# Performance work log

Measured on AMD Instinct MI355X. Metric: run time of the kernel, lower is better.

## Reference

```python
import jax, jax.numpy as jnp
import numpy as np

BIG = 1e9      # stand-in for +inf (keeps fp math/grad clean)
ALPHA = 0.5    # distillation weight from __init__
EPS = 1e-12


def _pairwise_dist(X):
    # Euclidean cdist: [N, d] -> [N, N]
    sq = jnp.sum(X * X, axis=1)
    D2 = sq[:, None] + sq[None, :] - 2.0 * (X @ X.T)
    return jnp.sqrt(jnp.maximum(D2, EPS))


def _h0_diagram(X):
    """0-dim persistence diagram from pairwise distances (single-linkage).
    births are 0, deaths are the sorted MST edge weights (Prim's algorithm).
    Returns [N-1, 2] (birth, death) pairs."""
    D = _pairwise_dist(X)           # [N, N]
    n = D.shape[0]
    visited0 = jnp.zeros(n, dtype=bool).at[0].set(True)

    def step(carry, _):
        dist, visited = carry       # dist: min distance from tree to each node
        masked = jnp.where(visited, BIG, dist)
        j = jnp.argmin(masked)
        w = masked[j]               # MST edge weight added this step
        visited = visited.at[j].set(True)
        dist = jnp.minimum(dist, D[j])
        return (dist, visited), w

    (_, _), deaths = jax.lax.scan(step, (D[0], visited0), None, length=n - 1)
    deaths = jnp.sort(deaths)
    return jnp.stack([jnp.zeros_like(deaths), deaths], axis=-1)  # [N-1, 2]


def reference(student_repr, teacher_repr, student_edges, teacher_edges):
    # representation MSE
    repr_loss = jnp.mean((student_repr - teacher_repr) ** 2)
    # topological distillation: MSE between H0 persistence diagrams
    # (edges are unused: persistence is computed from the feature distance matrix,
    #  matching ph.compute_from_distance(features) in the source)
    diag_s = _h0_diagram(student_repr)
    diag_t = _h0_diagram(teacher_repr)
    topo_loss = jnp.mean((diag_s - diag_t) ** 2)
    total = ALPHA * repr_loss + (1.0 - ALPHA) * topo_loss
    return total, repr_loss, topo_loss


def setup_inputs() -> dict:
    key = jax.random.key(0)
    k1, k2, k3, k4 = jax.random.split(key, 4)
    N, d, E = 4096, 128, 131072
    return {
        "student_repr": jax.random.normal(k1, (N, d), dtype=jnp.float32),
        "teacher_repr": jax.random.normal(k2, (N, d), dtype=jnp.float32),
        "student_edges": jax.random.randint(k3, (2, E), 0, N, dtype=jnp.int64)
        if jax.config.jax_enable_x64 else jax.random.randint(k3, (2, E), 0, N).astype(jnp.int32),
        "teacher_edges": jax.random.randint(k4, (2, E), 0, N, dtype=jnp.int64)
        if jax.config.jax_enable_x64 else jax.random.randint(k4, (2, E), 0, N).astype(jnp.int32),
    }
```

## Files before the change

kernel.cpp:

```cpp
#include <hip/hip_runtime.h>
#include <hip/hip_fp16.h>

#define N_NODES 4096
#define DIMS 128

typedef __attribute__((ext_vector_type(8))) short short8;
typedef __attribute__((ext_vector_type(4))) float f32x4;

static constexpr float BIGF = 1e9f;
static constexpr float EPSF = 1e-12f;
static constexpr unsigned long long KEY_INF = ~0ull;
static constexpr unsigned U32_INF = 0xFFFFFFFFu;


__device__ inline unsigned short f32_to_bf16(float f) {
    unsigned u = __float_as_uint(f);
    unsigned r = (u + 0x7FFFu + ((u >> 16) & 1u)) >> 16;
    return (unsigned short)r;
}

__device__ inline float half_bits_to_f32(unsigned short b) {
    __half h;
    __builtin_memcpy(&h, &b, 2);
    return __half2float(h);
}

__device__ inline unsigned u32min(unsigned a, unsigned b) { return a < b ? a : b; }

__device__ inline unsigned long long u64min(unsigned long long a, unsigned long long b) {
    return a < b ? a : b;
}

__device__ inline unsigned long long shfl_xor_u64(unsigned long long v, int m) {
    int lo = __shfl_xor((int)(unsigned)(v & 0xFFFFFFFFull), m);
    int hi = __shfl_xor((int)(unsigned)(v >> 32), m);
    return ((unsigned long long)(unsigned)hi << 32) | (unsigned)lo;
}

__device__ inline unsigned wave_min_u32(unsigned v) {
    #pragma unroll
    for (int s = 32; s; s >>= 1) v = u32min(v, (unsigned)__shfl_xor((int)v, s));
    return v;
}

__device__ inline float block_reduce_sum_256(float v) {
    __shared__ float s[4];
    __syncthreads();
    #pragma unroll
    for (int off = 32; off; off >>= 1) v += __shfl_xor(v, off);
    if ((threadIdx.x & 63) == 0) s[threadIdx.x >> 6] = v;
    __syncthreads();
    return s[0] + s[1] + s[2] + s[3];
}

__global__ __launch_bounds__(256) void prep_kernel(const float* __restrict__ S,
                                                   const float* __restrict__ T,
                                                   unsigned short* __restrict__ X16s,
                                                   unsigned short* __restrict__ X16t,
                                                   float* __restrict__ sqs,
                                                   float* __restrict__ sqt,
                                                   float* __restrict__ partials,
                                                   unsigned short* __restrict__ comp0,
                                                   unsigned long long* __restrict__ best_row,
                                                   unsigned* __restrict__ cnt,
                                                   unsigned* __restrict__ done,
                                                   unsigned* __restrict__ sctl) {
    const int t = threadIdx.x;
    const int gid = blockIdx.x * 256 + t;
    if (gid < 2 * N_NODES) {
        comp0[gid] = (unsigned short)(gid & (N_NODES - 1));
        best_row[gid] = KEY_INF;
    }
    if (gid < 2) { cnt[gid] = 0; done[gid] = 0; }
    if (gid == 0) sctl[0] = 0;

    const int wave = t >> 6, lane = t & 63;
    const int row = blockIdx.x * 8 + wave * 2 + (lane >> 5);
    const int c4 = (lane & 31) * 4;
    const size_t off = (size_t)row * DIMS + c4;
    float4 a = *(const float4*)&S[off];
    float4 b = *(const float4*)&T[off];
    float sa = a.x * a.x + a.y * a.y + a.z * a.z + a.w * a.w;
    float sb = b.x * b.x + b.y * b.y + b.z * b.z + b.w * b.w;
    #pragma unroll
    for (int m = 16; m; m >>= 1) { sa += __shfl_xor(sa, m); sb += __shfl_xor(sb, m); }
    if ((lane & 31) == 0) { sqs[row] = sa; sqt[row] = sb; }
    ushort4 oa, ob;
    oa.x = f32_to_bf16(a.x); oa.y = f32_to_bf16(a.y);
    oa.z = f32_to_bf16(a.z); oa.w = f32_to_bf16(a.w);
    ob.x = f32_to_bf16(b.x); ob.y = f32_to_bf16(b.y);
    ob.z = f32_to_bf16(b.z); ob.w = f32_to_bf16(b.w);
    *(ushort4*)&X16s[off] = oa;
    *(ushort4*)&X16t[off] = ob;
    float dx = a.x - b.x, dy = a.y - b.y, dz = a.z - b.z, dw = a.w - b.w;
    float rs = block_reduce_sum_256(dx * dx + dy * dy + dz * dz + dw * dw);
    if (t == 0) partials[blockIdx.x] = rs;
}

__global__ __launch_bounds__(256) void dist_kernel(const unsigned short* __restrict__ X16s,
                                                   const unsigned short* __restrict__ X16t,
                                                   const float* __restrict__ sqs,
                                                   const float* __restrict__ sqt,
                                                   __half* __restrict__ Ds,
                                                   __half* __restrict__ Dt,
                                                   unsigned long long* __restrict__ best_row,
                                                   unsigned* __restrict__ rowtile) {
    const int bi = blockIdx.y * 64;
    const int bj = blockIdx.x * 64;
    if (bj < bi) return;
    const int m = blockIdx.z;
    const unsigned short* __restrict__ X16 = m ? X16t : X16s;
    const float* __restrict__ sq = m ? sqt : sqs;
    unsigned short* __restrict__ D = (unsigned short*)(m ? Dt : Ds);
    unsigned long long* br = best_row + m * N_NODES;
    unsigned* rt = rowtile + (size_t)m * N_NODES * 64;

    __shared__ __align__(16) unsigned short Abuf[64 * 128];
    __shared__ __align__(16) unsigned short Bbuf[64 * 128];
    __shared__ unsigned colminLDS[4 * 64];
    unsigned short* tile16 = Abuf;

    const int t = threadIdx.x;

    #pragma unroll
    for (int p = 0; p < 4; p++) {
        int f = t + p * 256;
        int r = f >> 4, c8 = f & 15;
        int slot = c8 ^ (r & 7);
        uint4 va = *(const uint4*)&X16[(size_t)(bi + r) * DIMS + c8 * 8];
        *(uint4*)&Abuf[r * 128 + slot * 8] = va;
        uint4 vb = *(const uint4*)&X16[(size_t)(bj + r) * DIMS + c8 * 8];
        *(uint4*)&Bbuf[r * 128 + slot * 8] = vb;
    }
    __syncthreads();

    const int wave = t >> 6, lane = t & 63;
    const int l15 = lane & 15, kg = lane >> 4;

    const int rowA = wave * 16 + l15;
    short8 afrag[4];
    #pragma unroll
    for (int s = 0; s < 4; s++) {
        int c8 = s * 4 + kg;
        int slot = c8 ^ (rowA & 7);
        afrag[s] = *(const short8*)&Abuf[rowA * 128 + slot * 8];
    }
    __syncthreads();

    f32x4 acc[4] = {};
    #pragma unroll
    for (int n = 0; n < 4; n++) {
        const int rowB = n * 16 + l15;
        #pragma unroll
        for (int s = 0; s < 4; s++) {
            int c8 = s * 4 + kg;
            int slot = c8 ^ (rowB & 7);
            short8 bfrag = *(const short8*)&Bbuf[rowB * 128 + slot * 8];
            acc[n] = __builtin_amdgcn_mfma_f32_16x16x32_bf16(afrag[s], bfrag, acc[n], 0, 0, 0);
        }
    }

    const int r0 = wave * 16 + kg * 4;
    float sqi[4];
    #pragma unroll
    for (int rr = 0; rr < 4; rr++) sqi[rr] = sq[bi + r0 + rr];

    unsigned rowmin[4] = {U32_INF, U32_INF, U32_INF, U32_INF};
    unsigned colmin[4] = {U32_INF, U32_INF, U32_INF, U32_INF};
    #pragma unroll
    for (int n = 0; n < 4; n++) {
        const int col = bj + n * 16 + l15;
        const float sqj = sq[col];
        #pragma unroll
        for (int rr = 0; rr < 4; rr++) {
            float d2 = sqi[rr] + sqj - 2.0f * acc[n][rr];
            float dd = sqrtf(fmaxf(d2, EPSF));
            unsigned hb = (unsigned)__half_as_ushort(__float2half(dd));
            const int cc = n * 16 + l15;
            const int R = r0 + rr;
            tile16[R * 72 + ((((cc >> 3) ^ (R & 7)) << 3) | (cc & 7))] = (unsigned short)hb;
            if ((bi + R) != col) {
                rowmin[rr] = u32min(rowmin[rr], (hb << 12) | (unsigned)col);
                colmin[n]  = u32min(colmin[n],  (hb << 12) | (unsigned)R);
            }
        }
    }
    #pragma unroll
    for (int rr = 0; rr < 4; rr++) {
        unsigned k = rowmin[rr];
        #pragma unroll
        for (int s = 8; s; s >>= 1) k = u32min(k, (unsigned)__shfl_xor((int)k, s));
        if (l15 == 0) {
            const unsigned row = (unsigned)(bi + r0 + rr);
            rt[(size_t)row * 64 + (bj >> 6)] = k;
            unsigned j = k & 0xFFFu, d16 = k >> 12;
            unsigned a = row < j ? row : j, b2 = row < j ? j : row;
            atomicMin(&br[row],
                ((unsigned long long)d16 << 24) | ((unsigned long long)a << 12) | b2);
        }
    }
    #pragma unroll
    for (int n = 0; n < 4; n++) {
        unsigned k = colmin[n];
        k = u32min(k, (unsigned)__shfl_xor((int)k, 16));
        k = u32min(k, (unsigned)__shfl_xor((int)k, 32));
        if (kg == 0) colminLDS[wave * 64 + n * 16 + l15] = k;
    }
    __syncthreads();

    #pragma unroll
    for (int q = 0; q < 2; q++) {
        int lin = t * 2 + q;
        int r = lin >> 3, k8 = lin & 7;
        uint4 v = *(const uint4*)&tile16[r * 72 + ((k8 ^ (r & 7)) << 3)];
        *(uint4*)&D[(size_t)(bi + r) * N_NODES + bj + k8 * 8] = v;
    }
    if (bi != bj) {
        #pragma unroll
        for (int q = 0; q < 2; q++) {
            int lin = t * 2 + q;
            int c = lin >> 3, r8 = lin & 7;
            const int csl = ((c >> 3) << 3);
            unsigned w[4];
            #pragma unroll
            for (int h = 0; h < 4; h++) {
                int R0 = r8 * 8 + h * 2;
                int R1 = R0 + 1;
                unsigned lo = tile16[R0 * 72 + ((((c >> 3) ^ (R0 & 7)) << 3) | (c & 7))];
                unsigned hi = tile16[R1 * 72 + ((((c >> 3) ^ (R1 & 7)) << 3) | (c & 7))];
                w[h] = lo | (hi << 16);
            }
            uint4 v = make_uint4(w[0], w[1], w[2], w[3]);
            *(uint4*)&D[(size_t)(bj + c) * N_NODES + bi + r8 * 8] = v;
        }
        if (t < 64) {
            unsigned k = colminLDS[t];
            k = u32min(k, colminLDS[64 + t]);
            k = u32min(k, colminLDS[128 + t]);
            k = u32min(k, colminLDS[192 + t]);
            unsigned d16 = k >> 12, lrow = k & 0xFFFu;
            rt[(size_t)(bj + t) * 64 + (bi >> 6)] = (d16 << 12) | (unsigned)(bi + lrow);
            unsigned long long key64 = ((unsigned long long)d16 << 24) |
                ((unsigned long long)(bi + lrow) << 12) | (unsigned)(bj + t);
            atomicMin(&br[bj + t], key64);
        }
    }
}

__global__ __launch_bounds__(1024) void boruvka_merge2(
        const unsigned short* __restrict__ comp_in,
        unsigned short* __restrict__ comp_out,
        const unsigned long long* __restrict__ bc_in,
        unsigned long long* __restrict__ bc_out,
        const unsigned long long* __restrict__ best_row,
        unsigned short* __restrict__ wlist,
        unsigned* __restrict__ wcount,
        float* __restrict__ deaths,
        unsigned* __restrict__ cnt,
        unsigned* __restrict__ done) {
    const int m = blockIdx.x;
    if (done[m]) return;
    const unsigned short* cin = comp_in + m * N_NODES;
    const unsigned long long* bi = bc_in + m * N_NODES;
    const unsigned long long* br = best_row + m * N_NODES;
    float* dth = deaths + m * N_NODES;

    __shared__ unsigned short s_mc[N_NODES];
    __shared__ unsigned short s_mp[N_NODES];
    __shared__ unsigned long long s_bc[N_NODES];
    __shared__ unsigned s_wc;

    const int t = threadIdx.x;
    for (int i = t; i < N_NODES; i += 1024) {
        s_mc[i] = cin[i];
        s_mp[i] = (unsigned short)i;
        s_bc[i] = bi[i];
    }
    if (t == 0) s_wc = 0;
    __syncthreads();

    for (int i = t; i < N_NODES; i += 1024) {
        unsigned long long k = s_bc[i];
        if (k != KEY_INF) {
            unsigned canon = (unsigned)(k & 0xFFFFFFu);
            unsigned a = canon >> 12, b = canon & 0xFFFu;
            unsigned ca = s_mc[a], cb = s_mc[b];
            unsigned other = (ca == (unsigned)i) ? cb : ca;
            s_mp[i] = (unsigned short)other;
            bool mutual = (s_bc[other] == k);
            if (!mutual || (unsigned)i < other) {
                unsigned idx = atomicAdd(&cnt[m], 1u);
                dth[idx] = half_bits_to_f32((unsigned short)(k >> 24));
            }
        }
    }
    __syncthreads();

    unsigned nv[4];
    #pragma unroll
    for (int q = 0; q < 4; q++) {
        unsigned i = (unsigned)(t + q * 1024);
        unsigned p = s_mp[i], pp = s_mp[p];
        nv[q] = (pp == i) ? (i < p ? i : p) : p;
    }
    __syncthreads();
    #pragma unroll
    for (int q = 0; q < 4; q++) s_mp[t + q * 1024] = (unsigned short)nv[q];
    __syncthreads();

    #pragma unroll
    for (int q = 0; q < 4; q++) {
        unsigned rt = (unsigned)(t + q * 1024);
        unsigned p = s_mp[rt];
        while (p != rt) { rt = p; p = s_mp[rt]; }
        nv[q] = rt;
    }
    __syncthreads();
    #pragma unroll
    for (int q = 0; q < 4; q++) s_mp[t + q * 1024] = (unsigned short)nv[q];
    __syncthreads();

    #pragma unroll
    for (int q = 0; q < 4; q++) {
        int i = t + q * 1024;
        s_mc[i] = s_mp[s_mc[i]];
        s_bc[i] = KEY_INF;
    }
    __syncthreads();

    for (int i = t; i < N_NODES; i += 1024) {
        unsigned long long k = br[i];
        if (k != KEY_INF) {
            unsigned canon = (unsigned)(k & 0xFFFFFFu);
            unsigned a = canon >> 12, b = canon & 0xFFFu;
            unsigned j = (a == (unsigned)i) ? b : a;
            unsigned ci = s_mc[i];
            if (s_mc[j] != ci) {
                atomicMin(&s_bc[ci], k);
            } else {
                unsigned idx = atomicAdd(&s_wc, 1u);
                wlist[m * N_NODES + idx] = (unsigned short)i;
            }
        }
    }
    __syncthreads();

    for (int i = t; i < N_NODES; i += 1024) {
        comp_out[m * N_NODES + i] = s_mc[i];
        bc_out[m * N_NODES + i] = s_bc[i];
    }
    if (t == 0) {
        wcount[m] = s_wc;
        unsigned c = atomicAdd(&cnt[m], 0u);
        if (c >= N_NODES - 1) done[m] = 1u;
    }
}

__global__ __launch_bounds__(1024) void boruvka_scanw(
        const unsigned short* __restrict__ D0,
        const unsigned short* __restrict__ D1,
        const unsigned short* __restrict__ comp16,
        const unsigned short* __restrict__ wlist,
        const unsigned* __restrict__ wcount,
        unsigned* __restrict__ rowtile,
        unsigned long long* __restrict__ best_row,
        unsigned long long* __restrict__ bc_scan,
        const unsigned* __restrict__ done) {
    const int m = blockIdx.y;
    if (done[m]) return;
    const unsigned count = wcount[m];
    if (blockIdx.x * 16 >= count) return;

    const unsigned short* __restrict__ D = m ? D1 : D0;
    const unsigned short* cm = comp16 + m * N_NODES;
    unsigned* rt = rowtile + (size_t)m * N_NODES * 64;
    unsigned long long* br = best_row + m * N_NODES;
    unsigned long long* bc = bc_scan + m * N_NODES;

    __shared__ __align__(16) unsigned short s_c16[N_NODES];

    const int t = threadIdx.x;
    {
        uint2 v = ((const uint2*)cm)[t];
        *(uint2*)&s_c16[t * 4] = v;
    }
    __syncthreads();

    const int wave = t >> 6, lane = t & 63;
    const unsigned idx = blockIdx.x * 16 + wave;
    if (idx >= count) return;
    const int r = (int)wlist[m * N_NODES + idx];
    const unsigned short ci16 = s_c16[r];

    const unsigned short* row = D + (size_t)r * N_NODES;
    unsigned* rtr = rt + (size_t)r * 64;
    unsigned tm = rtr[lane];
    unsigned long long bcv = bc[ci16];

    unsigned tmin = wave_min_u32(tm);
    if (bcv != KEY_INF && (tmin >> 12) > (unsigned)(bcv >> 24)) return;

    unsigned avail = tm;
    unsigned sel;
    sel = ((avail >> 12) << 6) | (unsigned)lane;
    sel = wave_min_u32(sel);
    const int t0 = (int)(sel & 63);
    if (lane == t0) avail = U32_INF;
    sel = ((avail >> 12) << 6) | (unsigned)lane;
    sel = wave_min_u32(sel);
    const int t1 = (int)(sel & 63);
    if (lane == t1) avail = U32_INF;
    sel = ((avail >> 12) << 6) | (unsigned)lane;
    sel = wave_min_u32(sel);
    const int t2 = (int)(sel & 63);
    if (lane == t2) avail = U32_INF;
    sel = ((avail >> 12) << 6) | (unsigned)lane;
    sel = wave_min_u32(sel);
    const int t3 = (int)(sel & 63);

    unsigned short dv0 = row[t0 * 64 + lane];
    unsigned short dv1 = row[t1 * 64 + lane];
    unsigned short dv2 = row[t2 * 64 + lane];
    unsigned short dv3 = row[t3 * 64 + lane];
    unsigned short cv0 = s_c16[t0 * 64 + lane];
    unsigned short cv1 = s_c16[t1 * 64 + lane];
    unsigned short cv2 = s_c16[t2 * 64 + lane];
    unsigned short cv3 = s_c16[t3 * 64 + lane];
    unsigned F0 = wave_min_u32((cv0 != ci16) ? (((unsigned)dv0 << 12) | (unsigned)(t0 * 64 + lane)) : U32_INF);
    unsigned F1 = wave_min_u32((cv1 != ci16) ? (((unsigned)dv1 << 12) | (unsigned)(t1 * 64 + lane)) : U32_INF);
    unsigned F2 = wave_min_u32((cv2 != ci16) ? (((unsigned)dv2 << 12) | (unsigned)(t2 * 64 + lane)) : U32_INF);
    unsigned F3 = wave_min_u32((cv3 != ci16) ? (((unsigned)dv3 << 12) | (unsigned)(t3 * 64 + lane)) : U32_INF);
    unsigned B = u32min(u32min(F0, F1), u32min(F2, F3));
    if (lane == 0) { rtr[t0] = F0; rtr[t1] = F1; rtr[t2] = F2; rtr[t3] = F3; }
    if (lane == t0) tm = F0;
    if (lane == t1) tm = F1;
    if (lane == t2) tm = F2;
    if (lane == t3) tm = F3;

    unsigned long long need = __ballot(tm < B);
    if (need) {
        if (__popcll(need) > 6) {
            unsigned best32 = B;
            const unsigned cirep = (unsigned)ci16 | ((unsigned)ci16 << 16);
            #pragma unroll 4
            for (int it = 0; it < 8; it++) {
                const int e0 = it * 512 + lane * 8;
                uint4 dvv = *(const uint4*)&row[e0];
                uint4 cvv = *(const uint4*)&s_c16[e0];
                unsigned px = cvv.x ^ cirep, py = cvv.y ^ cirep;
                unsigned pz = cvv.z ^ cirep, pw = cvv.w ^ cirep;
                if (px | py | pz | pw) {
                    unsigned dws[4] = {dvv.x, dvv.y, dvv.z, dvv.w};
                    unsigned pp[4] = {px, py, pz, pw};
                    #pragma unroll
                    for (int h = 0; h < 4; h++) {
                        unsigned j0 = (unsigned)(e0 + h * 2);
                        if (pp[h] & 0xFFFFu)
                            best32 = u32min(best32, ((dws[h] & 0xFFFFu) << 12) | j0);
                        if (pp[h] >> 16)
                            best32 = u32min(best32, ((dws[h] >> 16) << 12) | (j0 + 1));
                    }
                }
            }
            B = wave_min_u32(best32);
        } else {
            while (need) {
                const int tl = __ffsll((unsigned long long)need) - 1;
                need &= need - 1;
                unsigned bnd = (unsigned)__shfl((int)tm, tl);
                if (bnd >= B) continue;
                unsigned short dv = row[tl * 64 + lane];
                unsigned short cv = s_c16[tl * 64 + lane];
                unsigned f = wave_min_u32((cv != ci16)
                    ? (((unsigned)dv << 12) | (unsigned)(tl * 64 + lane)) : U32_INF);
                if (lane == 0) rtr[tl] = f;
                B = u32min(B, f);
            }
        }
    }

    unsigned long long cached;
    if (B != U32_INF) {
        unsigned j = B & 0xFFFu, d16 = B >> 12;
        unsigned a = (unsigned)r < j ? (unsigned)r : j;
        unsigned b2 = (unsigned)r < j ? j : (unsigned)r;
        cached = ((unsigned long long)d16 << 24) | ((unsigned long long)a << 12) | b2;
    } else {
        cached = KEY_INF;
    }
    if (lane == 0) {
        br[r] = cached;
        if (cached != KEY_INF) atomicMin(&bc[ci16], cached);
    }
}

__device__ inline void tail_process_mask(unsigned long long mask, int rowbase,
                                         const unsigned short* __restrict__ D,
                                         unsigned* __restrict__ rt,
                                         unsigned short* s_c,
                                         unsigned long long* s_br,
                                         unsigned long long* s_bc,
                                         int lane) {
    while (mask) {
        const int l = __ffsll(mask) - 1; mask &= mask - 1;
        const int r = rowbase + l;
        const unsigned short ci16 = s_c[r];
        unsigned* rtr = rt + (size_t)r * 64;
        unsigned tm = rtr[lane];
        unsigned tmin = wave_min_u32(tm);
        unsigned long long bcv = s_bc[ci16];
        if (bcv != KEY_INF && (tmin >> 12) > (unsigned)(bcv >> 24)) continue;
        const unsigned short* row = D + (size_t)r * N_NODES;
        bool scanned = false;
        unsigned B = U32_INF;
        for (int it = 0; it < 64; ++it) {
            unsigned long long my =
                ((unsigned long long)(scanned ? U32_INF : tm) << 8) | (unsigned)lane;
            #pragma unroll
            for (int s = 32; s; s >>= 1) my = u64min(my, shfl_xor_u64(my, s));
            unsigned wtm = (unsigned)(my >> 8);
            if (wtm >= B) break;
            const int tl = (int)(my & 0xFFu);
            unsigned short dv = row[tl * 64 + lane];
            unsigned short cv = s_c[tl * 64 + lane];
            unsigned f = wave_min_u32((cv != ci16)
                ? (((unsigned)dv << 12) | (unsigned)(tl * 64 + lane)) : U32_INF);
            if (lane == tl) { scanned = true; tm = f; }
            if (lane == 0) rtr[tl] = f;
            B = u32min(B, f);
        }
        if (lane == 0) {
            if (B != U32_INF) {
                unsigned j = B & 0xFFFu, d16 = B >> 12;
                unsigned a = (unsigned)r < j ? (unsigned)r : j;
                unsigned b2 = (unsigned)r < j ? j : (unsigned)r;
                unsigned long long key = ((unsigned long long)d16 << 24) |
                    ((unsigned long long)a << 12) | b2;
                s_br[r] = key;
                atomicMin(&s_bc[ci16], key);
            } else {
                s_br[r] = KEY_INF;
            }
        }
    }
}

__global__ __launch_bounds__(1024) void boruvka_tail(const unsigned short* __restrict__ D0,
                                                     const unsigned short* __restrict__ D1,
                                                     unsigned short* __restrict__ comp16,
                                                     unsigned* __restrict__ rowtile,
                                                     unsigned long long* __restrict__ best_row,
                                                     float* __restrict__ deaths,
                                                     unsigned* __restrict__ cnt,
                                                     unsigned* __restrict__ done) {
    const int m = blockIdx.x;
    if (done[m]) return;
    const unsigned short* __restrict__ D = m ? D1 : D0;
    unsigned* rt = rowtile + (size_t)m * N_NODES * 64;
    float* dth = deaths + m * N_NODES;

    __shared__ unsigned short s_c[N_NODES];
    __shared__ unsigned short s_mp[N_NODES];
    __shared__ unsigned long long s_br[N_NODES];
    __shared__ unsigned long long s_bc[N_NODES];
    __shared__ unsigned s_cnt;

    const int t = threadIdx.x;
    const int wave = t >> 6, lane = t & 63;

    for (int i = t; i < N_NODES; i += 1024) {
        s_c[i] = comp16[m * N_NODES + i];
        s_br[i] = best_row[m * N_NODES + i];
        s_bc[i] = KEY_INF;
    }
    if (t == 0) s_cnt = cnt[m];
    __syncthreads();

    for (int round = 0; round < 16; ++round) {
        unsigned long long pend[4];
        #pragma unroll
        for (int b = 0; b < 4; b++) {
            const int rr = wave * 256 + b * 64 + lane;
            unsigned long long k = s_br[rr];
            bool need = false;
            if (k != KEY_INF) {
                unsigned canon = (unsigned)(k & 0xFFFFFFu);
                unsigned a = canon >> 12, bb = canon & 0xFFFu;
                unsigned j = (a == (unsigned)rr) ? bb : a;
                if (s_c[j] == s_c[rr]) need = true;
                else atomicMin(&s_bc[s_c[rr]], k);
            }
            pend[b] = __ballot(need);
            s_mp[rr] = (unsigned short)rr;
        }
        __syncthreads();

        #pragma unroll
        for (int b = 0; b < 4; b++)
            tail_process_mask(pend[b], wave * 256 + b * 64, D, rt, s_c, s_br, s_bc, lane);
        __syncthreads();

        for (int i = t; i < N_NODES; i += 1024) {
            unsigned long long k = s_bc[i];
            if (k != KEY_INF) {
                unsigned canon = (unsigned)(k & 0xFFFFFFu);
                unsigned a = canon >> 12, b = canon & 0xFFFu;
                unsigned ca = s_c[a], cb = s_c[b];
                unsigned other = (ca == (unsigned)i) ? cb : ca;
                s_mp[i] = (unsigned short)other;
                bool mutual = (s_bc[other] == k);
                if (!mutual || (unsigned)i < other) {
                    unsigned idx = atomicAdd(&s_cnt, 1u);
                    dth[idx] = half_bits_to_f32((unsigned short)(k >> 24));
                }
            }
        }
        __syncthreads();

        unsigned nv[4];
        #pragma unroll
        for (int q = 0; q < 4; q++) {
            unsigned i = (unsigned)(t + q * 1024);
            unsigned p = s_mp[i], pp = s_mp[p];
            nv[q] = (pp == i) ? (i < p ? i : p) : p;
        }
        __syncthreads();
        #pragma unroll
        for (int q = 0; q < 4; q++) s_mp[t + q * 1024] = (unsigned short)nv[q];
        __syncthreads();
        #pragma unroll
        for (int q = 0; q < 4; q++) {
            unsigned rr = (unsigned)(t + q * 1024);
            unsigned p = s_mp[rr];
            while (p != rr) { rr = p; p = s_mp[rr]; }
            nv[q] = rr;
        }
        __syncthreads();
        #pragma unroll
        for (int q = 0; q < 4; q++) s_mp[t + q * 1024] = (unsigned short)nv[q];
        __syncthreads();

        for (int i = t; i < N_NODES; i += 1024) {
            s_c[i] = s_mp[s_c[i]];
            s_bc[i] = KEY_INF;
        }
        __syncthreads();
        if (s_cnt >= N_NODES - 1) break;
    }

    for (int i = t; i < N_NODES; i += 1024) {
        comp16[m * N_NODES + i] = s_c[i];
        best_row[m * N_NODES + i] = s_br[i];
    }
    if (t == 0) {
        cnt[m] = s_cnt;
        if (s_cnt >= N_NODES - 1) done[m] = 1u;
    }
}

__global__ __launch_bounds__(1024) void sortfinal_kernel(float* __restrict__ deaths,
                                                         const float* __restrict__ partials,
                                                         unsigned* __restrict__ sctl,
                                                         float* __restrict__ out) {
    float* d = deaths + blockIdx.x * N_NODES;
    __shared__ float s[N_NODES];
    __shared__ float red[16], red2[16];
    __shared__ int s_last;
    const int t = threadIdx.x;
    if (t == 0) s_last = 0;
    for (int i = t; i < N_NODES - 1; i += 1024) s[i] = d[i];
    if (t == 0) s[N_NODES - 1] = BIGF;
    __syncthreads();

    {
        float v[4];
        #pragma unroll
        for (int q = 0; q < 4; q++) v[q] = s[t + q * 1024];
        #pragma unroll
        for (int k = 2; k <= 32; k <<= 1) {
            for (int j = k >> 1; j; j >>= 1) {
                #pragma unroll
                for (int q = 0; q < 4; q++) {
                    float o = __shfl_xor(v[q], j);
                    bool up  = (t & j) == 0;
                    bool asc = (((t + q * 1024) & k) == 0);
                    float lo = fminf(v[q], o), hi = fmaxf(v[q], o);
                    v[q] = (asc == up) ? lo : hi;
                }
            }
        }
        #pragma unroll
        for (int q = 0; q < 4; q++) s[t + q * 1024] = v[q];
    }
    __syncthreads();

    for (int k = 64; k <= N_NODES; k <<= 1) {
        for (int j = k >> 1; j >= 64; j >>= 1) {
            #pragma unroll
            for (int q = 0; q < 4; q++) {
                int i = t + q * 1024;
                int p = i ^ j;
                if (p > i) {
                    float a = s[i], b = s[p];
                    bool asc = (i & k) == 0;
                    if ((a > b) == asc) { s[i] = b; s[p] = a; }
                }
            }
            __syncthreads();
        }
        float v[4];
        #pragma unroll
        for (int q = 0; q < 4; q++) v[q] = s[t + q * 1024];
        for (int j = 32; j; j >>= 1) {
            #pragma unroll
            for (int q = 0; q < 4; q++) {
                float o = __shfl_xor(v[q], j);
                bool up  = (t & j) == 0;
                bool asc = (((t + q * 1024) & k) == 0);
                float lo = fminf(v[q], o), hi = fmaxf(v[q], o);
                v[q] = (asc == up) ? lo : hi;
            }
        }
        #pragma unroll
        for (int q = 0; q < 4; q++) s[t + q * 1024] = v[q];
        __syncthreads();
    }
    for (int i = t; i < N_NODES - 1; i += 1024) d[i] = s[i];

    __threadfence();
    __syncthreads();
    if (t == 0) {
        unsigned old = atomicAdd(sctl, 1u);
        if (old == 1) s_last = 1;
    }
    __syncthreads();
    if (!s_last) return;
    __threadfence();

    float a = 0.f;
    for (int i = t; i < N_NODES - 1; i += 1024) {
        float x = __uint_as_float(atomicAdd((unsigned*)&deaths[i], 0u));
        float y = __uint_as_float(atomicAdd((unsigned*)&deaths[N_NODES + i], 0u));
        float dd = x - y;
        a += dd * dd;
    }
    float rsum = (t < 512) ? partials[t] : 0.f;
    #pragma unroll
    for (int off = 32; off; off >>= 1) { a += __shfl_xor(a, off); rsum += __shfl_xor(rsum, off); }
    if ((t & 63) == 0) { red[t >> 6] = a; red2[t >> 6] = rsum; }
    __syncthreads();
    if (t == 0) {
        float topo_sum = 0.f, repr_sum = 0.f;
        #pragma unroll
        for (int i = 0; i < 16; i++) { topo_sum += red[i]; repr_sum += red2[i]; }
        float repr = repr_sum / (float)(N_NODES * DIMS);
        float topo = topo_sum / (float)(2 * (N_NODES - 1));
        out[0] = 0.5f * repr + 0.5f * topo;
        out[1] = repr;
        out[2] = topo;
    }
}


extern "C" void kernel_launch(void* const* d_in, const int* in_sizes, int n_in,
                              void* d_out, int out_size, void* d_ws, size_t ws_size,
                              hipStream_t stream) {
    const float* S = (const float*)d_in[0];
    const float* T = (const float*)d_in[1];
    float* out = (float*)d_out;

    const size_t nn = (size_t)N_NODES * N_NODES;
    char* p = (char*)d_ws;
    __half* Ds = (__half*)p;                   p += nn * 2;
    __half* Dt = (__half*)p;                   p += nn * 2;
    unsigned short* X16s = (unsigned short*)p; p += (size_t)N_NODES * DIMS * 2;
    unsigned short* X16t = (unsigned short*)p; p += (size_t)N_NODES * DIMS * 2;
    unsigned long long* bcA = (unsigned long long*)p; p += (size_t)2 * N_NODES * 8;
    unsigned long long* bcB = (unsigned long long*)p; p += (size_t)2 * N_NODES * 8;
    unsigned long long* best_row = (unsigned long long*)p; p += 2 * N_NODES * 8;
    unsigned* rowtile  = (unsigned*)p; p += (size_t)2 * N_NODES * 64 * 4;
    float*    sqs      = (float*)p;    p += N_NODES * 4;
    float*    sqt      = (float*)p;    p += N_NODES * 4;
    float*    deaths   = (float*)p;    p += 2 * N_NODES * 4;
    float*    partials = (float*)p;    p += 512 * 4;
    unsigned short* cb0 = (unsigned short*)p; p += 2 * N_NODES * 2;
    unsigned short* cb1 = (unsigned short*)p; p += 2 * N_NODES * 2;
    unsigned short* wlist = (unsigned short*)p; p += 2 * N_NODES * 2;
    unsigned* wcount   = (unsigned*)p; p += 2 * 4;
    unsigned* cnt      = (unsigned*)p; p += 2 * 4;
    unsigned* done     = (unsigned*)p; p += 2 * 4;
    unsigned* sctl     = (unsigned*)p;

    unsigned long long* bcbuf[2] = { bcA, bcB };
    unsigned short* cbuf[2] = { cb0, cb1 };

    prep_kernel<<<N_NODES / 8, 256, 0, stream>>>(S, T, X16s, X16t, sqs, sqt, partials,
                                                 cb0, best_row, cnt, done, sctl);

    dim3 dg(N_NODES / 64, N_NODES / 64, 2);
    dist_kernel<<<dg, 256, 0, stream>>>(X16s, X16t, sqs, sqt, Ds, Dt, best_row, rowtile);

    boruvka_merge2<<<2, 1024, 0, stream>>>(cb0, cb1, best_row, bcbuf[1], best_row,
                                           wlist, wcount, deaths, cnt, done);

    dim3 sg(N_NODES / 16, 2);
    for (int k = 1; k <= 5; k++) {
        boruvka_scanw<<<sg, 1024, 0, stream>>>((const unsigned short*)Ds,
                                               (const unsigned short*)Dt,
                                               cbuf[k & 1], wlist, wcount, rowtile,
                                               best_row, bcbuf[k & 1], done);
        boruvka_merge2<<<2, 1024, 0, stream>>>(cbuf[k & 1], cbuf[(k + 1) & 1],
                                               bcbuf[k & 1], bcbuf[(k + 1) & 1], best_row,
                                               wlist, wcount, deaths, cnt, done);
    }
    boruvka_tail<<<2, 1024, 0, stream>>>((const unsigned short*)Ds,
                                         (const unsigned short*)Dt,
                                         cb0, rowtile, best_row, deaths, cnt, done);
    sortfinal_kernel<<<2, 1024, 0, stream>>>(deaths, partials, sctl, out);
}
```

Measured before the change: 163.4 us.

## Split K-loop into two 64-wide halves and store squared distances in fp16

The distance kernel now stages the 128-dim inputs in two 64-column halves, with smaller A/B shared buffers and a dedicated output tile. This lowers shared-memory use per block, which can raise occupancy, at the cost of an extra barrier and a second load phase. It also drops the per-element sqrt: the matrix stores squared distances in fp16 and takes the sqrt only when a death value is emitted, which relies on sqrt being monotone so the MST ordering is unchanged. Storing d^2 in fp16 gives different rounding and ties than storing d, and large squared distances use more of the fp16 range.

```diff
diff --git a/kernel.cpp b/kernel.cpp
--- a/kernel.cpp
+++ b/kernel.cpp
@@ -19,10 +19,10 @@
     return (unsigned short)r;
 }
 
-__device__ inline float half_bits_to_f32(unsigned short b) {
+__device__ inline float half_bits_to_death(unsigned short b) {
     __half h;
     __builtin_memcpy(&h, &b, 2);
-    return __half2float(h);
+    return sqrtf(__half2float(h));
 }
 
 __device__ inline unsigned u32min(unsigned a, unsigned b) { return a < b ? a : b; }
@@ -115,48 +115,49 @@
     unsigned long long* br = best_row + m * N_NODES;
     unsigned* rt = rowtile + (size_t)m * N_NODES * 64;
 
-    __shared__ __align__(16) unsigned short Abuf[64 * 128];
-    __shared__ __align__(16) unsigned short Bbuf[64 * 128];
+    __shared__ __align__(16) unsigned short Abuf[64 * 64];
+    __shared__ __align__(16) unsigned short Bbuf[64 * 64];
+    __shared__ __align__(16) unsigned short tile16[64 * 72];
     __shared__ unsigned colminLDS[4 * 64];
-    unsigned short* tile16 = Abuf;
 
     const int t = threadIdx.x;
-
-    #pragma unroll
-    for (int p = 0; p < 4; p++) {
-        int f = t + p * 256;
-        int r = f >> 4, c8 = f & 15;
-        int slot = c8 ^ (r & 7);
-        uint4 va = *(const uint4*)&X16[(size_t)(bi + r) * DIMS + c8 * 8];
-        *(uint4*)&Abuf[r * 128 + slot * 8] = va;
-        uint4 vb = *(const uint4*)&X16[(size_t)(bj + r) * DIMS + c8 * 8];
-        *(uint4*)&Bbuf[r * 128 + slot * 8] = vb;
-    }
-    __syncthreads();
-
     const int wave = t >> 6, lane = t & 63;
     const int l15 = lane & 15, kg = lane >> 4;
 
-    const int rowA = wave * 16 + l15;
-    short8 afrag[4];
-    #pragma unroll
-    for (int s = 0; s < 4; s++) {
-        int c8 = s * 4 + kg;
-        int slot = c8 ^ (rowA & 7);
-        afrag[s] = *(const short8*)&Abuf[rowA * 128 + slot * 8];
-    }
-    __syncthreads();
-
     f32x4 acc[4] = {};
     #pragma unroll
-    for (int n = 0; n < 4; n++) {
-        const int rowB = n * 16 + l15;
-        #pragma unroll
-        for (int s = 0; s < 4; s++) {
-            int c8 = s * 4 + kg;
-            int slot = c8 ^ (rowB & 7);
-            short8 bfrag = *(const short8*)&Bbuf[rowB * 128 + slot * 8];
-            acc[n] = __builtin_amdgcn_mfma_f32_16x16x32_bf16(afrag[s], bfrag, acc[n], 0, 0, 0);
+    for (int half = 0; half < 2; half++) {
+        const int koff = half * 64;
+        if (half) __syncthreads();
+        #pragma unroll
+        for (int p = 0; p < 2; p++) {
+            int f = t + p * 256;
+            int r = f >> 3, c8 = f & 7;
+            int slot = c8 ^ (r & 7);
+            uint4 va = *(const uint4*)&X16[(size_t)(bi + r) * DIMS + koff + c8 * 8];
+            *(uint4*)&Abuf[r * 64 + slot * 8] = va;
+            uint4 vb = *(const uint4*)&X16[(size_t)(bj + r) * DIMS + koff + c8 * 8];
+            *(uint4*)&Bbuf[r * 64 + slot * 8] = vb;
+        }
+        __syncthreads();
+
+        const int rowA = wave * 16 + l15;
+        short8 af0, af1;
+        {
+            int c8 = 0 * 4 + kg;
+            af0 = *(const short8*)&Abuf[rowA * 64 + (c8 ^ (rowA & 7)) * 8];
+            c8 = 1 * 4 + kg;
+            af1 = *(const short8*)&Abuf[rowA * 64 + (c8 ^ (rowA & 7)) * 8];
+        }
+        #pragma unroll
+        for (int n = 0; n < 4; n++) {
+            const int rowB = n * 16 + l15;
+            int c8 = 0 * 4 + kg;
+            short8 bf0 = *(const short8*)&Bbuf[rowB * 64 + (c8 ^ (rowB & 7)) * 8];
+            acc[n] = __builtin_amdgcn_mfma_f32_16x16x32_bf16(af0, bf0, acc[n], 0, 0, 0);
+            c8 = 1 * 4 + kg;
+            short8 bf1 = *(const short8*)&Bbuf[rowB * 64 + (c8 ^ (rowB & 7)) * 8];
+            acc[n] = __builtin_amdgcn_mfma_f32_16x16x32_bf16(af1, bf1, acc[n], 0, 0, 0);
         }
     }
 
@@ -174,8 +175,7 @@
         #pragma unroll
         for (int rr = 0; rr < 4; rr++) {
             float d2 = sqi[rr] + sqj - 2.0f * acc[n][rr];
-            float dd = sqrtf(fmaxf(d2, EPSF));
-            unsigned hb = (unsigned)__half_as_ushort(__float2half(dd));
+            unsigned hb = (unsigned)__half_as_ushort(__float2half(fmaxf(d2, EPSF)));
             const int cc = n * 16 + l15;
             const int R = r0 + rr;
             tile16[R * 72 + ((((cc >> 3) ^ (R & 7)) << 3) | (cc & 7))] = (unsigned short)hb;
@@ -220,7 +220,6 @@
         for (int q = 0; q < 2; q++) {
             int lin = t * 2 + q;
             int c = lin >> 3, r8 = lin & 7;
-            const int csl = ((c >> 3) << 3);
             unsigned w[4];
             #pragma unroll
             for (int h = 0; h < 4; h++) {
@@ -290,7 +289,7 @@
             bool mutual = (s_bc[other] == k);
             if (!mutual || (unsigned)i < other) {
                 unsigned idx = atomicAdd(&cnt[m], 1u);
-                dth[idx] = half_bits_to_f32((unsigned short)(k >> 24));
+                dth[idx] = half_bits_to_death((unsigned short)(k >> 24));
             }
         }
     }
@@ -611,7 +610,7 @@
                 bool mutual = (s_bc[other] == k);
                 if (!mutual || (unsigned)i < other) {
                     unsigned idx = atomicAdd(&s_cnt, 1u);
-                    dth[idx] = half_bits_to_f32((unsigned short)(k >> 24));
+                    dth[idx] = half_bits_to_death((unsigned short)(k >> 24));
                 }
             }
         }
```

New measurement: 157.0 us (median of 2 runs). 1.04x faster.
